# Kernel tuning notes

Hardware: AMD Instinct MI355X
Metric: run time of the kernel (lower is better)

The kernel has to match this reference:

```python
import jax, jax.numpy as jnp
import numpy as np
from jax import lax

H = 250  # hidden size of all LSTM layers


def _lstm_layer(x, Wih, Whh, bih, bhh):
    """Single-layer LSTM over time-major x [T, in], batch=1 folded away.
    PyTorch gate order: i, f, g, o. Returns hidden states [T, H]."""
    b = bih + bhh
    # Precompute input projections for all timesteps (parallel GEMM)
    xW = x @ Wih.T + b  # [T, 4H]

    def step(carry, xw_t):
        h, c = carry
        gates = xw_t + h @ Whh.T  # [4H]
        i, f, g, o = jnp.split(gates, 4)
        i = jax.nn.sigmoid(i)
        f = jax.nn.sigmoid(f)
        g = jnp.tanh(g)
        o = jax.nn.sigmoid(o)
        c = f * c + i * g
        h = o * jnp.tanh(c)
        return (h, c), h

    h0 = jnp.zeros((Whh.shape[1],), x.dtype)
    (_, _), hs = lax.scan(step, (h0, h0), xW)
    return hs  # [T, H]


def setup_inputs() -> dict:
    key = jax.random.key(0)
    ks = jax.random.split(key, 16)
    T, D = 8192, 1
    s = 1.0 / np.sqrt(H)  # PyTorch default uniform(-1/sqrt(H), 1/sqrt(H))
    u = lambda k, shape: jax.random.uniform(k, shape, jnp.float32, -s, s)
    inp = {
        "input_seq": jax.random.normal(ks[0], (T, D), jnp.float32),
        # lstm (2 layers), layer 0: input_size=1
        "Wih0": u(ks[1], (4 * H, D)), "Whh0": u(ks[2], (4 * H, H)),
        "bih0": u(ks[3], (4 * H,)), "bhh0": u(ks[4], (4 * H,)),
        # lstm layer 1: input=H
        "Wih1": u(ks[5], (4 * H, H)), "Whh1": u(ks[6], (4 * H, H)),
        "bih1": u(ks[7], (4 * H,)), "bhh1": u(ks[8], (4 * H,)),
        # lstm_1 (1 layer): input=H
        "Wih2": u(ks[9], (4 * H, H)), "Whh2": u(ks[10], (4 * H, H)),
        "bih2": u(ks[11], (4 * H,)), "bhh2": u(ks[12], (4 * H,)),
        # final linear H -> 1
        "Wl": u(ks[13], (1, H)), "bl": u(ks[14], (1,)),
    }
    return inp


def reference(input_seq, Wih0, Whh0, bih0, bhh0, Wih1, Whh1, bih1, bhh1,
              Wih2, Whh2, bih2, bhh2, Wl, bl):
    T = input_seq.shape[0]
    x = input_seq.reshape(T, -1)            # [T, 1] (batch=1 squeezed)
    h0 = _lstm_layer(x, Wih0, Whh0, bih0, bhh0)   # stacked LSTM layer 0
    h1 = _lstm_layer(h0, Wih1, Whh1, bih1, bhh1)  # layer 1 (dropout=0.2 inactive at eval)
    h2 = _lstm_layer(h1, Wih2, Whh2, bih2, bhh2)  # second LSTM module
    preds = h2 @ Wl.T + bl                  # [T, 1]
    return preds[-1]                        # [1]
```

## Files before the change

kernel.cpp:

```cpp
#include <hip/hip_runtime.h>
#include <cstdint>

#define HDIM 250
#define GDIM 1000
#define CH   64
#define PP   4
#define NW   4
#define HRING 4
#define XRING 4
#define RPAD 1024
#define NTH  1024

#define HSEG 144
#define HBUF (4 * HSEG)
#define HB_BASE 32768
#define RED_BASE (HB_BASE + 2 * HBUF)
#define SMEM_BYTES 92160

typedef _Float16 f16x2 __attribute__((ext_vector_type(2)));

__device__ __forceinline__ float fdot2u(uint32_t w, uint32_t h, float acc) {
#if defined(__has_builtin) && __has_builtin(__builtin_amdgcn_fdot2)
  return __builtin_amdgcn_fdot2(__builtin_bit_cast(f16x2, w),
                                __builtin_bit_cast(f16x2, h), acc, false);
#else
  f16x2 wv = __builtin_bit_cast(f16x2, w), hv = __builtin_bit_cast(f16x2, h);
  return acc + (float)wv[0] * (float)hv[0] + (float)wv[1] * (float)hv[1];
#endif
}

__device__ __forceinline__ uint32_t pkh2(float a, float b) {
  f16x2 p; p[0] = (_Float16)a; p[1] = (_Float16)b;
  return __builtin_bit_cast(uint32_t, p);
}

__device__ __forceinline__ uint4 pack8q(const float* rp, int c0) {
  float c[8];
#pragma unroll
  for (int u = 0; u < 8; ++u) {
    int col = c0 + u;
    c[u] = (rp && col < HDIM) ? rp[col] : 0.f;
  }
  uint4 r;
  r.x = pkh2(c[0], c[1]); r.y = pkh2(c[2], c[3]);
  r.z = pkh2(c[4], c[5]); r.w = pkh2(c[6], c[7]);
  return r;
}

__device__ __forceinline__ float rcpf_(float x) {
#if defined(__has_builtin) && __has_builtin(__builtin_amdgcn_rcpf)
  return __builtin_amdgcn_rcpf(x);
#else
  return 1.f / x;
#endif
}
__device__ __forceinline__ float sigm(float x) {
  return rcpf_(1.f + exp2f(-1.44269504088896341f * x));
}
__device__ __forceinline__ float tanh_(float x) {
  float e = exp2f(2.88539008177792681f * x);
  return 1.f - 2.f * rcpf_(e + 1.f);
}

template <int CTRL>
__device__ __forceinline__ float dppq(float v) {
  return __builtin_bit_cast(
      float, __builtin_amdgcn_update_dpp(0, __builtin_bit_cast(int, v), CTRL,
                                         0xF, 0xF, true));
}
template <int IMM>
__device__ __forceinline__ float swz(float v) {
  return __builtin_bit_cast(
      float, __builtin_amdgcn_ds_swizzle(__builtin_bit_cast(int, v), IMM));
}

__device__ __forceinline__ void step_barrier() {
  asm volatile("s_waitcnt lgkmcnt(0)\n\ts_barrier" ::: "memory");
}

#define F_HCNTW(F, li, w)  (F)[(li) * 4 + (w)]
#define F_XWCONW(F, li, w) (F)[8 + (li) * 4 + (w)]
#define F_HDONE(F, li, p)  (F)[16 + (li) * 4 + (p)]
#define F_XWRDY(F, li, c)  (F)[32 + (li) * 128 + (c)]
#define F_HXC(F, L, w)     (F)[512 + (L) * 4 + (w)]

__device__ __forceinline__ int aload(int* p) {
  return __hip_atomic_load(p, __ATOMIC_RELAXED, __HIP_MEMORY_SCOPE_AGENT);
}
__device__ __forceinline__ void arel(int* p, int v) {
  __hip_atomic_store(p, v, __ATOMIC_RELEASE, __HIP_MEMORY_SCOPE_AGENT);
}
__device__ __forceinline__ void acq_fence() {
  __builtin_amdgcn_fence(__ATOMIC_ACQUIRE, "agent");
}
__device__ __forceinline__ void spin_ge(int* p, int tgt) {
  unsigned n = 0;
  while (aload(p) < tgt) {
    __builtin_amdgcn_s_sleep(1);
    if (++n > 100000000u) return;
  }
}

__global__ void lstm_init(const float* __restrict__ Wih1, const float* __restrict__ bih1,
                          const float* __restrict__ bhh1, const float* __restrict__ Wih2,
                          const float* __restrict__ bih2, const float* __restrict__ bhh2,
                          float* __restrict__ WT, float* __restrict__ BV) {
  int idx = blockIdx.x * blockDim.x + threadIdx.x;
  int stride = gridDim.x * blockDim.x;
  for (int i = idx; i < 2 * HDIM * RPAD; i += stride) {
    int li = i / (HDIM * RPAD);
    int rem = i - li * HDIM * RPAD;
    int j = rem / RPAD, r = rem - j * RPAD;
    const float* W = li ? Wih2 : Wih1;
    WT[i] = (r < GDIM) ? W[r * HDIM + j] : 0.f;
  }
  for (int i = idx; i < 2 * RPAD; i += stride) {
    int li = i >> 10, r = i & 1023;
    const float* bi = li ? bih2 : bih1;
    const float* bh = li ? bhh2 : bhh1;
    BV[i] = (r < GDIM) ? bi[r] + bh[r] : 0.f;
  }
}

__global__ void __launch_bounds__(NTH) lstm_main(
    const float* __restrict__ x, const float* __restrict__ Wih0,
    const float* __restrict__ bih0, const float* __restrict__ bhh0,
    const float* __restrict__ Whh0, const float* __restrict__ Whh1,
    const float* __restrict__ Whh2, const float* __restrict__ Wl,
    const float* __restrict__ bl, int* __restrict__ F, float* __restrict__ hx,
    const float* __restrict__ WT, const float* __restrict__ BV,
    float* __restrict__ hRing, float* __restrict__ xwRing,
    float* __restrict__ out, int T) {
  __shared__ __align__(16) char smem[SMEM_BYTES];
  const int tid = threadIdx.x;
  const int bid = blockIdx.x;
  const int rem = bid & 7, grp = bid >> 3;
  const int NC = T / CH;

  if (rem < 3) {
    const int L = rem, w = grp;
    const int sl = tid & 3;
    const int gate = (tid >> 2) & 3;
    const int lu = tid >> 4;
    const int UW = (w < 3) ? 64 : 58;
    const int u_glob = w * 64 + lu;
    const bool uok = (lu < UW);
    const bool lead = ((tid & 15) == 0) && uok;
    const int r_abs = gate * HDIM + u_glob;

    const float* Whh = (L == 0) ? Whh0 : (L == 1) ? Whh1 : Whh2;
    const float* rp = uok ? (Whh + (size_t)r_abs * HDIM) : (const float*)nullptr;
    char* lw = smem + tid * 16;
#define LW(q) (lw + (size_t)(q) * (NTH * 16))

    uint4 q0 = pack8q(rp, sl * 64 + 0);
    uint4 q1 = pack8q(rp, sl * 64 + 8);
    uint4 q2 = pack8q(rp, sl * 64 + 16);
    uint4 q3 = pack8q(rp, sl * 64 + 24);
    uint4 q4 = pack8q(rp, sl * 64 + 32);
    uint4 q5 = pack8q(rp, sl * 64 + 40);
    *(uint4*)LW(0) = pack8q(rp, sl * 64 + 48);
    *(uint4*)LW(1) = pack8q(rp, sl * 64 + 56);

    float w0_ = 0.f, b0_ = 0.f;
    if (L == 0 && uok) {
      w0_ = Wih0[r_abs];
      b0_ = bih0[r_abs] + bhh0[r_abs];
    }

    const int lt = tid - 768;
    int cw = -1, li2 = 0;
    bool loader = false;
    if (lt >= 0 && lt < 96) {
      int idx = lt >> 5;
      li2 = lt & 31;
      cw = idx + (idx >= w ? 1 : 0);
      loader = li2 < ((cw == 3) ? 29 : 32);
    }

    for (int i = tid; i < (2 * HBUF) / 4; i += NTH)
      *(uint32_t*)(smem + HB_BASE + 4 * i) = 0u;
    __syncthreads();

    const float* xwBase = xwRing + (size_t)(L > 0 ? L - 1 : 0) * XRING * CH * RPAD;
    float* hBase = hRing + (size_t)L * HRING * CH * HDIM;
    float c_st = 0.f;

    for (int tt = 0; tt < T; ++tt) {
      const int tc = tt & (CH - 1);
      const int c = tt >> 6;
      const int p = tt & 1, ns = p ^ 1;
      if (tc == 0) {
        if (tid == 0) {
          if (L > 0) spin_ge(&F_XWRDY(F, L - 1, c), 1);
          if (L < 2 && c >= HRING) {
            int cc = c - HRING;
            spin_ge(&F_HDONE(F, L, cc % PP), cc + 1);
          }
          acq_fence();
        }
        __syncthreads();
      }

      float xw = 0.f;
      if (uok) {
        if (L == 0) {
          xw = fmaf(x[tt], w0_, b0_);
        } else {
          const float* xp = xwBase + (size_t)(c & (XRING - 1)) * CH * RPAD +
                            (size_t)tc * RPAD;
          xw = xp[r_abs];
        }
      }

      const char* hbp = smem + HB_BASE + p * HBUF + sl * HSEG;
      float a = 0.f;
#define FD4(W_, H_)                  \
  a = fdot2u((W_).x, (H_).x, a);     \
  a = fdot2u((W_).y, (H_).y, a);     \
  a = fdot2u((W_).z, (H_).z, a);     \
  a = fdot2u((W_).w, (H_).w, a);
      { uint4 hq = *(const uint4*)(hbp + 0);  FD4(q0, hq) }
      { uint4 hq = *(const uint4*)(hbp + 16); FD4(q1, hq) }
      { uint4 hq = *(const uint4*)(hbp + 32); FD4(q2, hq) }
      { uint4 hq = *(const uint4*)(hbp + 48); FD4(q3, hq) }
      { uint4 hq = *(const uint4*)(hbp + 64); FD4(q4, hq) }
      { uint4 hq = *(const uint4*)(hbp + 80); FD4(q5, hq) }
      { uint4 hq = *(const uint4*)(hbp + 96);  uint4 t6 = *(const uint4*)LW(0); FD4(t6, hq) }
      { uint4 hq = *(const uint4*)(hbp + 112); uint4 t7 = *(const uint4*)LW(1); FD4(t7, hq) }

      a += dppq<0xB1>(a);
      a += dppq<0x4E>(a);
      a += xw;

      float v4 = swz<0x101F>(a);
      float v8 = swz<0x201F>(a);
      float vc = swz<0x301F>(a);
      const float gi = (gate == 0) ? a : (gate == 1) ? v4 : (gate == 2) ? v8 : vc;
      const float gf = ((gate ^ 1) == 0) ? a : ((gate ^ 1) == 1) ? v4 : ((gate ^ 1) == 2) ? v8 : vc;
      const float gG = ((gate ^ 2) == 0) ? a : ((gate ^ 2) == 1) ? v4 : ((gate ^ 2) == 2) ? v8 : vc;
      const float go = ((gate ^ 3) == 0) ? a : ((gate ^ 3) == 1) ? v4 : ((gate ^ 3) == 2) ? v8 : vc;

      const float ii = sigm(gi), ff = sigm(gf), tg = tanh_(gG), oo = sigm(go);
      c_st = ff * c_st + ii * tg;
      const float hn = oo * tanh_(c_st);

      if (lead) {
        if (L < 2)
          hBase[(size_t)(c & (HRING - 1)) * CH * HDIM + (size_t)tc * HDIM + u_glob] = hn;
        __hip_atomic_store((uint32_t*)&hx[(L * 2 + ns) * 256 + u_glob],
                           __builtin_bit_cast(uint32_t, hn), __ATOMIC_RELAXED,
                           __HIP_MEMORY_SCOPE_AGENT);
      }
      asm volatile("s_waitcnt vmcnt(0)" ::: "memory");
      __syncthreads();
      if (tid == 0) {
        arel(&F_HXC(F, L, w), tt + 1);
        if (tc == CH - 1) {
          if (L < 2) arel(&F_HCNTW(F, L, w), c + 1);
          if (L > 0) arel(&F_XWCONW(F, L - 1, w), c + 1);
        }
      }

      if (lead)
        *(_Float16*)(smem + HB_BASE + ns * HBUF + (u_glob >> 6) * HSEG +
                     (u_glob & 63) * 2) = (_Float16)hn;
      if (loader) {
        spin_ge(&F_HXC(F, L, cw), tt + 1);
        acq_fence();
        const float2 hv = *(const float2*)&hx[(L * 2 + ns) * 256 + 64 * cw + 2 * li2];
        *(uint32_t*)(smem + HB_BASE + ns * HBUF + cw * HSEG + 4 * li2) =
            pkh2(hv.x, hv.y);
      }
      step_barrier();
    }

    if (L == 2 && w == 0) {
      float* red = (float*)(smem + RED_BASE);
      const int pT = T & 1;
      if (tid < HDIM) {
        float hv = (float)*(_Float16*)(smem + HB_BASE + pT * HBUF +
                                       (tid >> 6) * HSEG + (tid & 63) * 2);
        red[tid] = hv * Wl[tid];
      }
      __syncthreads();
      if (tid == 0) {
        float s = bl[0];
        for (int j = 0; j < HDIM; ++j) s += red[j];
        out[0] = s;
      }
    }
  } else if (rem == 4 || rem == 5) {
    const int li = rem - 4;
    const int p = grp;
    float* ldsH = (float*)smem;
    const int lane = tid & 63, wid = tid >> 6;
    const float* WTl = WT + (size_t)li * HDIM * RPAD;
    const float* BVl = BV + (size_t)li * RPAD;

    for (int c = p; c < NC; c += PP) {
      if (tid == 0) {
        for (int ww = 0; ww < NW; ++ww) spin_ge(&F_HCNTW(F, li, ww), c + 1);
        if (c >= XRING)
          for (int ww = 0; ww < NW; ++ww)
            spin_ge(&F_XWCONW(F, li, ww), c - XRING + 1);
        acq_fence();
      }
      __syncthreads();
      const float* hsrc = hRing + (size_t)li * HRING * CH * HDIM +
                          (size_t)(c & (HRING - 1)) * CH * HDIM;
      for (int t = wid; t < CH; t += 16)
        for (int j = lane; j < HDIM; j += 64)
          ldsH[t * 257 + j] = hsrc[t * HDIM + j];
      __syncthreads();
      if (tid == 0) arel(&F_HDONE(F, li, p), c + 1);

      float* xdst = xwRing + (size_t)li * XRING * CH * RPAD +
                    (size_t)(c & (XRING - 1)) * CH * RPAD;
      const int rb0 = wid * 64;
      for (int grpq = 0; grpq < 8; ++grpq) {
        const int rb = rb0 + grpq * 8;
        float acc[8];
#pragma unroll
        for (int uq = 0; uq < 8; ++uq) acc[uq] = 0.f;
        const float* wp = WTl + rb;
        float4 wa4 = *(const float4*)(wp);
        float4 wb4 = *(const float4*)(wp + 4);
        for (int j = 0; j < HDIM; ++j) {
          int jn = (j + 1 < HDIM) ? j + 1 : HDIM - 1;
          float4 na = *(const float4*)(wp + (size_t)jn * RPAD);
          float4 nb = *(const float4*)(wp + (size_t)jn * RPAD + 4);
          float hj = ldsH[lane * 257 + j];
          acc[0] = fmaf(wa4.x, hj, acc[0]); acc[1] = fmaf(wa4.y, hj, acc[1]);
          acc[2] = fmaf(wa4.z, hj, acc[2]); acc[3] = fmaf(wa4.w, hj, acc[3]);
          acc[4] = fmaf(wb4.x, hj, acc[4]); acc[5] = fmaf(wb4.y, hj, acc[5]);
          acc[6] = fmaf(wb4.z, hj, acc[6]); acc[7] = fmaf(wb4.w, hj, acc[7]);
          wa4 = na; wb4 = nb;
        }
#pragma unroll
        for (int uq = 0; uq < 8; ++uq) {
          int r = rb + uq;
          if (r < GDIM) xdst[(size_t)lane * RPAD + r] = acc[uq] + BVl[r];
        }
      }
      __syncthreads();
      if (tid == 0) arel(&F_XWRDY(F, li, c), 1);
    }
  }
}

extern "C" void kernel_launch(void* const* d_in, const int* in_sizes, int n_in,
                              void* d_out, int out_size, void* d_ws, size_t ws_size,
                              hipStream_t stream) {
  const float* x    = (const float*)d_in[0];
  const float* Wih0 = (const float*)d_in[1];
  const float* Whh0 = (const float*)d_in[2];
  const float* bih0 = (const float*)d_in[3];
  const float* bhh0 = (const float*)d_in[4];
  const float* Wih1 = (const float*)d_in[5];
  const float* Whh1 = (const float*)d_in[6];
  const float* bih1 = (const float*)d_in[7];
  const float* bhh1 = (const float*)d_in[8];
  const float* Wih2 = (const float*)d_in[9];
  const float* Whh2 = (const float*)d_in[10];
  const float* bih2 = (const float*)d_in[11];
  const float* bhh2 = (const float*)d_in[12];
  const float* Wl   = (const float*)d_in[13];
  const float* bl   = (const float*)d_in[14];
  const int T = in_sizes[0];

  char* ws = (char*)d_ws;
  int*   F   = (int*)ws;
  float* hx  = (float*)(ws + 4096);
  float* WT  = (float*)(ws + 12288);
  float* BV  = (float*)(ws + 12288 + 2048000);
  float* hR  = (float*)(ws + 12288 + 2048000 + 8192);
  float* xwR = (float*)(ws + 12288 + 2048000 + 8192 + 512000);

  hipMemsetAsync(ws, 0, 12288, stream);
  lstm_init<<<256, 256, 0, stream>>>(Wih1, bih1, bhh1, Wih2, bih2, bhh2, WT, BV);
  lstm_main<<<32, NTH, 0, stream>>>(
      x, Wih0, bih0, bhh0, Whh0, Whh1, Whh2, Wl, bl, F, hx, WT, BV, hR, xwR,
      (float*)d_out, T);
}
```

Baseline: 23.06 ms.

## Replace per-step flag handshake with tagged 64-bit hidden-state words

Each LSTM workgroup now publishes its hidden-state pairs as packed fp16 values together with a timestep tag in a single 64-bit atomic store. Consumers spin directly on that tagged word, so the per-step release flag, the vmcnt wait, one __syncthreads and the acquire fence on the recurrent critical path all go away. The full flush and barrier now happen only at chunk boundaries. This relies on 64-bit atomic stores being seen whole, and on ds_swizzle pairing adjacent units correctly; the double-buffer index is no longer used for the global exchange, which leans on the tag for ordering.

```diff
diff --git a/kernel.cpp b/kernel.cpp
--- a/kernel.cpp
+++ b/kernel.cpp
@@ -82,7 +82,6 @@
 #define F_XWCONW(F, li, w) (F)[8 + (li) * 4 + (w)]
 #define F_HDONE(F, li, p)  (F)[16 + (li) * 4 + (p)]
 #define F_XWRDY(F, li, c)  (F)[32 + (li) * 128 + (c)]
-#define F_HXC(F, L, w)     (F)[512 + (L) * 4 + (w)]
 
 __device__ __forceinline__ int aload(int* p) {
   return __hip_atomic_load(p, __ATOMIC_RELAXED, __HIP_MEMORY_SCOPE_AGENT);
@@ -127,7 +126,8 @@
     const float* __restrict__ bih0, const float* __restrict__ bhh0,
     const float* __restrict__ Whh0, const float* __restrict__ Whh1,
     const float* __restrict__ Whh2, const float* __restrict__ Wl,
-    const float* __restrict__ bl, int* __restrict__ F, float* __restrict__ hx,
+    const float* __restrict__ bl, int* __restrict__ F,
+    unsigned long long* __restrict__ hx64,
     const float* __restrict__ WT, const float* __restrict__ BV,
     float* __restrict__ hRing, float* __restrict__ xwRing,
     float* __restrict__ out, int T) {
@@ -245,34 +245,46 @@
       c_st = ff * c_st + ii * tg;
       const float hn = oo * tanh_(c_st);
 
+      const float hOdd = swz<0x401F>(hn);
+
       if (lead) {
         if (L < 2)
           hBase[(size_t)(c & (HRING - 1)) * CH * HDIM + (size_t)tc * HDIM + u_glob] = hn;
-        __hip_atomic_store((uint32_t*)&hx[(L * 2 + ns) * 256 + u_glob],
-                           __builtin_bit_cast(uint32_t, hn), __ATOMIC_RELAXED,
-                           __HIP_MEMORY_SCOPE_AGENT);
-      }
-      asm volatile("s_waitcnt vmcnt(0)" ::: "memory");
-      __syncthreads();
-      if (tid == 0) {
-        arel(&F_HXC(F, L, w), tt + 1);
-        if (tc == CH - 1) {
+        *(_Float16*)(smem + HB_BASE + ns * HBUF + (u_glob >> 6) * HSEG +
+                     (u_glob & 63) * 2) = (_Float16)hn;
+        if (!(lu & 1)) {
+          unsigned long long word =
+              (unsigned long long)pkh2(hn, hOdd) |
+              ((unsigned long long)(unsigned)(tt + 1) << 32);
+          __hip_atomic_store(&hx64[L * 128 + (u_glob >> 1)], word,
+                             __ATOMIC_RELAXED, __HIP_MEMORY_SCOPE_AGENT);
+        }
+      }
+
+      if (loader) {
+        unsigned long long* src = &hx64[L * 128 + 32 * cw + li2];
+        unsigned long long word;
+        unsigned n = 0;
+        do {
+          word = __hip_atomic_load(src, __ATOMIC_RELAXED,
+                                   __HIP_MEMORY_SCOPE_AGENT);
+          if (++n > 50000000u) break;
+        } while ((unsigned)(word >> 32) < (unsigned)(tt + 1));
+        *(uint32_t*)(smem + HB_BASE + ns * HBUF + cw * HSEG + 4 * li2) =
+            (uint32_t)word;
+      }
+
+      if (tc == CH - 1) {
+        asm volatile("s_waitcnt vmcnt(0)" ::: "memory");
+        __syncthreads();
+        if (tid == 0) {
           if (L < 2) arel(&F_HCNTW(F, L, w), c + 1);
           if (L > 0) arel(&F_XWCONW(F, L - 1, w), c + 1);
         }
-      }
-
-      if (lead)
-        *(_Float16*)(smem + HB_BASE + ns * HBUF + (u_glob >> 6) * HSEG +
-                     (u_glob & 63) * 2) = (_Float16)hn;
-      if (loader) {
-        spin_ge(&F_HXC(F, L, cw), tt + 1);
-        acq_fence();
-        const float2 hv = *(const float2*)&hx[(L * 2 + ns) * 256 + 64 * cw + 2 * li2];
-        *(uint32_t*)(smem + HB_BASE + ns * HBUF + cw * HSEG + 4 * li2) =
-            pkh2(hv.x, hv.y);
-      }
-      step_barrier();
+        __syncthreads();
+      } else {
+        step_barrier();
+      }
     }
 
     if (L == 2 && w == 0) {
@@ -370,16 +382,16 @@
   const int T = in_sizes[0];
 
   char* ws = (char*)d_ws;
-  int*   F   = (int*)ws;
-  float* hx  = (float*)(ws + 4096);
-  float* WT  = (float*)(ws + 12288);
-  float* BV  = (float*)(ws + 12288 + 2048000);
-  float* hR  = (float*)(ws + 12288 + 2048000 + 8192);
-  float* xwR = (float*)(ws + 12288 + 2048000 + 8192 + 512000);
-
-  hipMemsetAsync(ws, 0, 12288, stream);
+  int* F = (int*)ws;
+  unsigned long long* hx64 = (unsigned long long*)(ws + 4096);
+  float* WT  = (float*)(ws + 8192);
+  float* BV  = (float*)(ws + 8192 + 2048000);
+  float* hR  = (float*)(ws + 8192 + 2048000 + 8192);
+  float* xwR = (float*)(ws + 8192 + 2048000 + 8192 + 512000);
+
+  hipMemsetAsync(ws, 0, 8192, stream);
   lstm_init<<<256, 256, 0, stream>>>(Wih1, bih1, bhh1, Wih2, bih2, bhh2, WT, BV);
   lstm_main<<<32, NTH, 0, stream>>>(
-      x, Wih0, bih0, bhh0, Whh0, Whh1, Whh2, Wl, bl, F, hx, WT, BV, hR, xwR,
+      x, Wih0, bih0, bhh0, Whh0, Whh1, Whh2, Wl, bl, F, hx64, WT, BV, hR, xwR,
       (float*)d_out, T);
 }
```

New measurement: 19.80 ms. -14.1%, faster.
